# Optimization experiments

Hardware: AMD Instinct MI355X
Metric: run time of the kernel (lower is better)

The kernel has to match this reference:

```python
import jax, jax.numpy as jnp
import numpy as np

EPS_PIXEL = 1e-8
EPS_INST = 1e-5  # torch InstanceNorm2d default
NEG_SLOPE = 0.2


def setup_inputs() -> dict:
    key = jax.random.key(0)
    k1, k2, k3, k4, k5, k6 = jax.random.split(key, 6)
    B, C, H, W, S = 16, 512, 64, 64, 512
    x = jax.random.normal(k1, (B, C, H, W), dtype=jnp.float32)
    noise = jax.random.normal(k2, (B, 1, H, W), dtype=jnp.float32)
    style = jax.random.normal(k3, (B, S), dtype=jnp.float32)
    # NoiseLayer weight initialized to zeros in torch; use small random to exercise grads
    noise_weight = jax.random.normal(k4, (C,), dtype=jnp.float32) * 0.1
    lin_W = jax.random.normal(k5, (S, 2 * C), dtype=jnp.float32) / jnp.sqrt(S).astype(jnp.float32)
    lin_b = jax.random.normal(k6, (2 * C,), dtype=jnp.float32) * 0.01
    return {"x": x, "noise": noise, "style": style,
            "noise_weight": noise_weight, "lin_W": lin_W, "lin_b": lin_b}


def reference(x, noise, style, noise_weight, lin_W, lin_b):
    # Noise: per-pixel noise, per-channel weight
    x = x + noise_weight[None, :, None, None] * noise  # [B,C,H,W]
    # Activation: LeakyReLU(0.2)
    x = jnp.where(x >= 0, x, NEG_SLOPE * x)
    # PixelNorm: normalize by RMS over channel dim
    x = x * jax.lax.rsqrt(jnp.mean(x * x, axis=1, keepdims=True) + EPS_PIXEL)
    # InstanceNorm2d (affine=False): normalize over spatial dims per (b, c)
    mean = jnp.mean(x, axis=(2, 3), keepdims=True)
    var = jnp.mean(jnp.square(x - mean), axis=(2, 3), keepdims=True)
    x = (x - mean) * jax.lax.rsqrt(var + EPS_INST)
    # StyleMod: linear -> [B, 2, C], scale-shift
    s = style @ lin_W + lin_b            # [B, 2C]
    s = s.reshape(x.shape[0], 2, x.shape[1], 1, 1)
    return x * (s[:, 0] + 1.0) + s[:, 1]
```

## Files before the change

kernel.cpp:

```cpp
#include <hip/hip_runtime.h>


#define BB 16
#define CC 512
#define HWN 4096
#define HW4 1024
#define KSPLIT 64
#define CPB (CC / KSPLIT)

#define EPS_PIXEL 1e-8f
#define EPS_INST 1e-5f

__global__ void style_gemm(const float* __restrict__ style,
                           const float* __restrict__ lin_W,
                           const float* __restrict__ lin_b,
                           float* __restrict__ s_lin) {
    const int b = blockIdx.x;
    const int j = blockIdx.y * 256 + threadIdx.x;
    __shared__ float ssty[512];
    ssty[threadIdx.x]       = style[b * 512 + threadIdx.x];
    ssty[threadIdx.x + 256] = style[b * 512 + 256 + threadIdx.x];
    __syncthreads();
    float acc = lin_b[j];
#pragma unroll 8
    for (int k = 0; k < 512; ++k)
        acc = fmaf(ssty[k], lin_W[k * 1024 + j], acc);
    s_lin[b * 1024 + j] = acc;
}

__global__ void pixel_partial(const float* __restrict__ x,
                              const float* __restrict__ noise,
                              const float* __restrict__ nw,
                              float* __restrict__ partial) {
    const int bid = blockIdx.x;
    const int b  = bid >> 6;
    const int cs = bid & 63;
    const int c0 = cs * CPB;
    const int t = threadIdx.x;

    const float4* x4 = (const float4*)x;
    const float4* n4 = (const float4*)noise + (size_t)b * HW4;

    float4 nz[4], acc[4];
#pragma unroll
    for (int i = 0; i < 4; ++i) {
        nz[i] = n4[t + 256 * i];
        acc[i] = make_float4(0.f, 0.f, 0.f, 0.f);
    }

#pragma unroll
    for (int cci = 0; cci < CPB; ++cci) {
        const int c = c0 + cci;
        const float w = nw[c];
        const float4* xp = x4 + (size_t)(b * CC + c) * HW4;
#pragma unroll
        for (int i = 0; i < 4; ++i) {
            float4 v = xp[t + 256 * i];
            float y0 = fmaf(w, nz[i].x, v.x); y0 = fmaxf(y0, 0.2f * y0);
            float y1 = fmaf(w, nz[i].y, v.y); y1 = fmaxf(y1, 0.2f * y1);
            float y2 = fmaf(w, nz[i].z, v.z); y2 = fmaxf(y2, 0.2f * y2);
            float y3 = fmaf(w, nz[i].w, v.w); y3 = fmaxf(y3, 0.2f * y3);
            acc[i].x = fmaf(y0, y0, acc[i].x);
            acc[i].y = fmaf(y1, y1, acc[i].y);
            acc[i].z = fmaf(y2, y2, acc[i].z);
            acc[i].w = fmaf(y3, y3, acc[i].w);
        }
    }

    float4* pp = (float4*)partial + (size_t)(b * KSPLIT + cs) * HW4;
#pragma unroll
    for (int i = 0; i < 4; ++i)
        pp[t + 256 * i] = acc[i];
}

__global__ void pixel_reduce(const float* __restrict__ partial,
                             float* __restrict__ rbuf) {
    const int g = blockIdx.x * 256 + threadIdx.x;
    const int b = g >> 10;
    const int q = g & 1023;
    const float4* p4 = (const float4*)partial;
    float4 s = make_float4(0.f, 0.f, 0.f, 0.f);
#pragma unroll 8
    for (int k = 0; k < KSPLIT; ++k) {
        float4 v = p4[(size_t)(b * KSPLIT + k) * HW4 + q];
        s.x += v.x; s.y += v.y; s.z += v.z; s.w += v.w;
    }
    const float inv_c = 1.0f / (float)CC;
    float4 o;
    o.x = rsqrtf(fmaf(s.x, inv_c, EPS_PIXEL));
    o.y = rsqrtf(fmaf(s.y, inv_c, EPS_PIXEL));
    o.z = rsqrtf(fmaf(s.z, inv_c, EPS_PIXEL));
    o.w = rsqrtf(fmaf(s.w, inv_c, EPS_PIXEL));
    ((float4*)rbuf)[g] = o;
}

__global__ void fused_apply(const float* __restrict__ x,
                            const float* __restrict__ noise,
                            const float* __restrict__ nw,
                            const float* __restrict__ rbuf,
                            const float* __restrict__ s_lin,
                            float* __restrict__ out) {
    const int bid = blockIdx.x;
    const int b = bid >> 9;
    const int c = bid & 511;
    const int t = threadIdx.x;
    const float w = nw[c];

    const float4* x4 = (const float4*)x + (size_t)(b * CC + c) * HW4;
    const float4* n4 = (const float4*)noise + (size_t)b * HW4;
    const float4* r4 = (const float4*)rbuf + (size_t)b * HW4;

    float4 z[4];
    float sum = 0.f, sum2 = 0.f;
#pragma unroll
    for (int i = 0; i < 4; ++i) {
        const int q = t + 256 * i;
        float4 v = x4[q];
        float4 nz = n4[q];
        float4 rr = r4[q];
        float y0 = fmaf(w, nz.x, v.x); y0 = fmaxf(y0, 0.2f * y0);
        float y1 = fmaf(w, nz.y, v.y); y1 = fmaxf(y1, 0.2f * y1);
        float y2 = fmaf(w, nz.z, v.z); y2 = fmaxf(y2, 0.2f * y2);
        float y3 = fmaf(w, nz.w, v.w); y3 = fmaxf(y3, 0.2f * y3);
        float4 zz;
        zz.x = y0 * rr.x; zz.y = y1 * rr.y; zz.z = y2 * rr.z; zz.w = y3 * rr.w;
        z[i] = zz;
        sum  += zz.x + zz.y + zz.z + zz.w;
        sum2 = fmaf(zz.x, zz.x, sum2);
        sum2 = fmaf(zz.y, zz.y, sum2);
        sum2 = fmaf(zz.z, zz.z, sum2);
        sum2 = fmaf(zz.w, zz.w, sum2);
    }

    __shared__ float lds[16];
#pragma unroll
    for (int off = 32; off > 0; off >>= 1) {
        sum  += __shfl_down(sum, off, 64);
        sum2 += __shfl_down(sum2, off, 64);
    }
    const int lane = t & 63, wv = t >> 6;
    if (lane == 0) { lds[wv] = sum; lds[8 + wv] = sum2; }
    __syncthreads();
    if (t == 0) {
        float S1 = lds[0] + lds[1] + lds[2] + lds[3];
        float S2 = lds[8] + lds[9] + lds[10] + lds[11];
        float m = S1 * (1.0f / (float)HWN);
        float var = fmaf(-m, m, S2 * (1.0f / (float)HWN));
        float istd = rsqrtf(var + EPS_INST);
        float s0 = s_lin[b * 1024 + c];
        float s1 = s_lin[b * 1024 + 512 + c];
        float A = istd * (s0 + 1.0f);
        lds[12] = A;
        lds[13] = fmaf(-m, A, s1);
    }
    __syncthreads();
    const float A = lds[12];
    const float Bs = lds[13];

    float4* o4 = (float4*)out + (size_t)(b * CC + c) * HW4;
#pragma unroll
    for (int i = 0; i < 4; ++i) {
        const int q = t + 256 * i;
        float4 zz = z[i];
        float4 o;
        o.x = fmaf(zz.x, A, Bs);
        o.y = fmaf(zz.y, A, Bs);
        o.z = fmaf(zz.z, A, Bs);
        o.w = fmaf(zz.w, A, Bs);
        o4[q] = o;
    }
}

extern "C" void kernel_launch(void* const* d_in, const int* in_sizes, int n_in,
                              void* d_out, int out_size, void* d_ws, size_t ws_size,
                              hipStream_t stream) {
    const float* x      = (const float*)d_in[0];
    const float* noise  = (const float*)d_in[1];
    const float* style  = (const float*)d_in[2];
    const float* nw     = (const float*)d_in[3];
    const float* lin_W  = (const float*)d_in[4];
    const float* lin_b  = (const float*)d_in[5];
    float* out = (float*)d_out;
    float* ws  = (float*)d_ws;

    float* s_lin = ws;
    float* rbuf  = ws + 16384;
    float* partial = out;

    style_gemm<<<dim3(BB, 4), 256, 0, stream>>>(style, lin_W, lin_b, s_lin);
    pixel_partial<<<BB * KSPLIT, 256, 0, stream>>>(x, noise, nw, partial);
    pixel_reduce<<<(BB * HW4) / 256, 256, 0, stream>>>(partial, rbuf);
    fused_apply<<<BB * CC, 256, 0, stream>>>(x, noise, nw, rbuf, s_lin, out);
}
```

Before: 304.0 us.

## Fuse style GEMM into partial kernel with K-split and restructure pixel reduce

```diff
diff --git a/kernel.cpp b/kernel.cpp
--- a/kernel.cpp
+++ b/kernel.cpp
@@ -7,36 +7,44 @@
 #define HW4 1024
 #define KSPLIT 64
 #define CPB (CC / KSPLIT)
+#define NSTYLE 256
 
 #define EPS_PIXEL 1e-8f
 #define EPS_INST 1e-5f
 
-__global__ void style_gemm(const float* __restrict__ style,
-                           const float* __restrict__ lin_W,
-                           const float* __restrict__ lin_b,
-                           float* __restrict__ s_lin) {
-    const int b = blockIdx.x;
-    const int j = blockIdx.y * 256 + threadIdx.x;
-    __shared__ float ssty[512];
-    ssty[threadIdx.x]       = style[b * 512 + threadIdx.x];
-    ssty[threadIdx.x + 256] = style[b * 512 + 256 + threadIdx.x];
-    __syncthreads();
-    float acc = lin_b[j];
+__global__ __launch_bounds__(256) void k1_partials(
+        const float* __restrict__ x,
+        const float* __restrict__ noise,
+        const float* __restrict__ nw,
+        const float* __restrict__ style,
+        const float* __restrict__ lin_W,
+        const float* __restrict__ lin_b,
+        float* __restrict__ partial,
+        float* __restrict__ sp) {
+    const int bid = blockIdx.x;
+    const int t = threadIdx.x;
+
+    if (bid < NSTYLE) {
+        const int b  = bid >> 4;
+        const int jg = (bid >> 2) & 3;
+        const int z  = bid & 3;
+        const int j  = jg * 256 + t;
+        __shared__ float ssty[128];
+        if (t < 128) ssty[t] = style[b * 512 + z * 128 + t];
+        __syncthreads();
+        float acc = (z == 0) ? lin_b[j] : 0.0f;
+        const float* Wp = lin_W + (size_t)(z * 128) * 1024 + j;
 #pragma unroll 8
-    for (int k = 0; k < 512; ++k)
-        acc = fmaf(ssty[k], lin_W[k * 1024 + j], acc);
-    s_lin[b * 1024 + j] = acc;
-}
-
-__global__ void pixel_partial(const float* __restrict__ x,
-                              const float* __restrict__ noise,
-                              const float* __restrict__ nw,
-                              float* __restrict__ partial) {
-    const int bid = blockIdx.x;
-    const int b  = bid >> 6;
-    const int cs = bid & 63;
+        for (int k = 0; k < 128; ++k)
+            acc = fmaf(ssty[k], Wp[(size_t)k * 1024], acc);
+        sp[(size_t)(b * 4 + z) * 1024 + j] = acc;
+        return;
+    }
+
+    const int pb = bid - NSTYLE;
+    const int b  = pb >> 6;
+    const int cs = pb & 63;
     const int c0 = cs * CPB;
-    const int t = threadIdx.x;
 
     const float4* x4 = (const float4*)x;
     const float4* n4 = (const float4*)noise + (size_t)b * HW4;
@@ -73,44 +81,71 @@
         pp[t + 256 * i] = acc[i];
 }
 
-__global__ void pixel_reduce(const float* __restrict__ partial,
-                             float* __restrict__ rbuf) {
-    const int g = blockIdx.x * 256 + threadIdx.x;
-    const int b = g >> 10;
-    const int q = g & 1023;
+__global__ __launch_bounds__(256) void pixel_reduce(
+        const float* __restrict__ partial,
+        float* __restrict__ rbuf) {
+    const int bid = blockIdx.x;
+    const int b  = bid >> 4;
+    const int qb = (bid & 15) * 64;
+    const int t = threadIdx.x;
+    const int ql = t & 63;
+    const int kq = t >> 6;
+
     const float4* p4 = (const float4*)partial;
     float4 s = make_float4(0.f, 0.f, 0.f, 0.f);
-#pragma unroll 8
-    for (int k = 0; k < KSPLIT; ++k) {
+    const int q = qb + ql;
+#pragma unroll
+    for (int kk = 0; kk < 16; ++kk) {
+        const int k = kq * 16 + kk;
         float4 v = p4[(size_t)(b * KSPLIT + k) * HW4 + q];
         s.x += v.x; s.y += v.y; s.z += v.z; s.w += v.w;
     }
-    const float inv_c = 1.0f / (float)CC;
-    float4 o;
-    o.x = rsqrtf(fmaf(s.x, inv_c, EPS_PIXEL));
-    o.y = rsqrtf(fmaf(s.y, inv_c, EPS_PIXEL));
-    o.z = rsqrtf(fmaf(s.z, inv_c, EPS_PIXEL));
-    o.w = rsqrtf(fmaf(s.w, inv_c, EPS_PIXEL));
-    ((float4*)rbuf)[g] = o;
-}
-
-__global__ void fused_apply(const float* __restrict__ x,
-                            const float* __restrict__ noise,
-                            const float* __restrict__ nw,
-                            const float* __restrict__ rbuf,
-                            const float* __restrict__ s_lin,
-                            float* __restrict__ out) {
+    __shared__ float4 red[256];
+    red[t] = s;
+    __syncthreads();
+    if (t < 64) {
+        float4 a0 = red[t], a1 = red[t + 64], a2 = red[t + 128], a3 = red[t + 192];
+        float sx = a0.x + a1.x + a2.x + a3.x;
+        float sy = a0.y + a1.y + a2.y + a3.y;
+        float sz = a0.z + a1.z + a2.z + a3.z;
+        float sw = a0.w + a1.w + a2.w + a3.w;
+        const float inv_c = 1.0f / (float)CC;
+        float4 o;
+        o.x = rsqrtf(fmaf(sx, inv_c, EPS_PIXEL));
+        o.y = rsqrtf(fmaf(sy, inv_c, EPS_PIXEL));
+        o.z = rsqrtf(fmaf(sz, inv_c, EPS_PIXEL));
+        o.w = rsqrtf(fmaf(sw, inv_c, EPS_PIXEL));
+        ((float4*)rbuf)[b * HW4 + qb + t] = o;
+    }
+}
+
+__global__ __launch_bounds__(256) void fused_apply(
+        const float* __restrict__ x,
+        const float* __restrict__ noise,
+        const float* __restrict__ nw,
+        const float* __restrict__ rbuf,
+        const float* __restrict__ sp,
+        float* __restrict__ out) {
     const int bid = blockIdx.x;
     const int b = bid >> 9;
     const int c = bid & 511;
     const int t = threadIdx.x;
     const float w = nw[c];
 
+    float s0p = 0.f, s1p = 0.f;
+    if (t == 0) {
+#pragma unroll
+        for (int z = 0; z < 4; ++z) {
+            s0p += sp[(size_t)(b * 4 + z) * 1024 + c];
+            s1p += sp[(size_t)(b * 4 + z) * 1024 + 512 + c];
+        }
+    }
+
     const float4* x4 = (const float4*)x + (size_t)(b * CC + c) * HW4;
     const float4* n4 = (const float4*)noise + (size_t)b * HW4;
     const float4* r4 = (const float4*)rbuf + (size_t)b * HW4;
 
-    float4 z[4];
+    float4 zv[4];
     float sum = 0.f, sum2 = 0.f;
 #pragma unroll
     for (int i = 0; i < 4; ++i) {
@@ -124,7 +159,7 @@
         float y3 = fmaf(w, nz.w, v.w); y3 = fmaxf(y3, 0.2f * y3);
         float4 zz;
         zz.x = y0 * rr.x; zz.y = y1 * rr.y; zz.z = y2 * rr.z; zz.w = y3 * rr.w;
-        z[i] = zz;
+        zv[i] = zz;
         sum  += zz.x + zz.y + zz.z + zz.w;
         sum2 = fmaf(zz.x, zz.x, sum2);
         sum2 = fmaf(zz.y, zz.y, sum2);
@@ -147,11 +182,9 @@
         float m = S1 * (1.0f / (float)HWN);
         float var = fmaf(-m, m, S2 * (1.0f / (float)HWN));
         float istd = rsqrtf(var + EPS_INST);
-        float s0 = s_lin[b * 1024 + c];
-        float s1 = s_lin[b * 1024 + 512 + c];
-        float A = istd * (s0 + 1.0f);
+        float A = istd * (s0p + 1.0f);
         lds[12] = A;
-        lds[13] = fmaf(-m, A, s1);
+        lds[13] = fmaf(-m, A, s1p);
     }
     __syncthreads();
     const float A = lds[12];
@@ -161,7 +194,7 @@
 #pragma unroll
     for (int i = 0; i < 4; ++i) {
         const int q = t + 256 * i;
-        float4 zz = z[i];
+        float4 zz = zv[i];
         float4 o;
         o.x = fmaf(zz.x, A, Bs);
         o.y = fmaf(zz.y, A, Bs);
@@ -183,12 +216,12 @@
     float* out = (float*)d_out;
     float* ws  = (float*)d_ws;
 
-    float* s_lin = ws;
-    float* rbuf  = ws + 16384;
+    float* sp   = ws;
+    float* rbuf = ws + 65536;
     float* partial = out;
 
-    style_gemm<<<dim3(BB, 4), 256, 0, stream>>>(style, lin_W, lin_b, s_lin);
-    pixel_partial<<<BB * KSPLIT, 256, 0, stream>>>(x, noise, nw, partial);
-    pixel_reduce<<<(BB * HW4) / 256, 256, 0, stream>>>(partial, rbuf);
-    fused_apply<<<BB * CC, 256, 0, stream>>>(x, noise, nw, rbuf, s_lin, out);
-}
+    k1_partials<<<NSTYLE + BB * KSPLIT, 256, 0, stream>>>(
+        x, noise, nw, style, lin_W, lin_b, partial, sp);
+    pixel_reduce<<<256, 256, 0, stream>>>(partial, rbuf);
+    fused_apply<<<BB * CC, 256, 0, stream>>>(x, noise, nw, rbuf, sp, out);
+}
```

After: 266.1 us. -12.5%, faster.
